# Optimization experiments

Hardware: AMD Instinct MI355X
Metric: run time of the kernel (lower is better)

## Reference

```python
import jax, jax.numpy as jnp
import numpy as np
import math

EPS = 1e-3  # numerical_stabilizer in relu_kernel_transformation


def setup_inputs() -> dict:
    key = jax.random.key(0)
    ks = jax.random.split(key, 6)
    B, L, DIM = 8, 4096, 768
    H, D, M = 12, 64, 256
    x = jax.random.normal(ks[0], (B, L, DIM), dtype=jnp.float32)
    qkv_w = jax.random.normal(ks[1], (3 * DIM, DIM), dtype=jnp.float32) * (DIM ** -0.5)
    qkv_b = jnp.zeros((3 * DIM,), dtype=jnp.float32)
    proj_w = jax.random.normal(ks[2], (DIM, DIM), dtype=jnp.float32) * (DIM ** -0.5)
    proj_b = jnp.zeros((DIM,), dtype=jnp.float32)
    # Gaussian orthogonal random matrix [M, D] (blocks of orthogonal rows, chi-scaled)
    blocks = []
    for i in range(M // D):
        g = jax.random.normal(ks[3 + 0] if False else jax.random.fold_in(ks[3], i), (D, D), dtype=jnp.float32)
        q, _ = jnp.linalg.qr(g)
        blocks.append(q.T)
    pm = jnp.concatenate(blocks, axis=0)  # [M, D]
    mult = jnp.linalg.norm(jax.random.normal(ks[4], (M, D), dtype=jnp.float32), axis=1)
    proj_mat = mult[:, None] * pm
    return {"x": x, "qkv_w": qkv_w, "qkv_b": qkv_b,
            "proj_w": proj_w, "proj_b": proj_b, "proj_mat": proj_mat}


def _relu_features(t, proj_mat):
    # t: [B, L, H, D], proj_mat: [M, D] -> [B, L, H, M]
    ratio = 1.0 / math.sqrt(float(proj_mat.shape[0]))
    z = ratio * jnp.einsum('blhd,md->blhm', t, proj_mat)
    return jax.nn.relu(z) + EPS


def reference(x, qkv_w, qkv_b, proj_w, proj_b, proj_mat):
    B, L, DIM = x.shape
    H = 12
    D = DIM // H
    qkv = x @ qkv_w.T + qkv_b                      # [B, L, 3*DIM]
    qkv = qkv.reshape(B, L, 3, H, D)
    q, k, v = qkv[:, :, 0], qkv[:, :, 1], qkv[:, :, 2]   # [B, L, H, D]
    q_p = _relu_features(q, proj_mat)              # [B, L, H, M]
    k_p = _relu_features(k, proj_mat)              # [B, L, H, M]
    # Non-causal FAVOR+ linear attention
    kv = jnp.einsum('blhm,blhd->bhmd', k_p, v)     # [B, H, M, D]
    k_sum = k_p.sum(axis=1)                        # [B, H, M]
    num = jnp.einsum('blhm,bhmd->blhd', q_p, kv)   # [B, L, H, D]
    den = jnp.einsum('blhm,bhm->blh', q_p, k_sum)  # [B, L, H]
    out = num / den[..., None]
    out = out.reshape(B, L, DIM)
    return out @ proj_w.T + proj_b
```

## Files before the change

kernel.cpp:

```cpp
#include <hip/hip_runtime.h>
#include <hip/hip_bf16.h>
#include <cstdint>

typedef __hip_bfloat16 bf16;
typedef short bf16x8 __attribute__((ext_vector_type(8)));
typedef float f32x4 __attribute__((ext_vector_type(4)));

#define RATIO 0.0625f
#define EPS_F 0.001f

__device__ __forceinline__ void unpack8(uint4 u, float* f) {
  f[0] = __uint_as_float(u.x << 16); f[1] = __uint_as_float(u.x & 0xffff0000u);
  f[2] = __uint_as_float(u.y << 16); f[3] = __uint_as_float(u.y & 0xffff0000u);
  f[4] = __uint_as_float(u.z << 16); f[5] = __uint_as_float(u.z & 0xffff0000u);
  f[6] = __uint_as_float(u.w << 16); f[7] = __uint_as_float(u.w & 0xffff0000u);
}

__device__ __forceinline__ unsigned short f2bf(float f) {
  unsigned int u = __float_as_uint(f);
  unsigned int r = (u + 0x7fffu + ((u >> 16) & 1u)) >> 16;
  return (unsigned short)r;
}

__device__ __forceinline__ void gload_lds16(const void* g, void* l) {
  __builtin_amdgcn_global_load_lds(
      (const __attribute__((address_space(1))) void*)(uintptr_t)g,
      (__attribute__((address_space(3))) void*)(uintptr_t)l, 16, 0, 0);
}

__global__ void conv_kernel(const float* __restrict__ src,
                            unsigned short* __restrict__ dst, long n) {
  long i = ((long)blockIdx.x * 256 + threadIdx.x) * 4;
  if (i < n) {
    float4 v = *(const float4*)(src + i);
    ushort4 o;
    o.x = f2bf(v.x); o.y = f2bf(v.y); o.z = f2bf(v.z); o.w = f2bf(v.w);
    *(ushort4*)(dst + i) = o;
  }
}

__device__ __forceinline__ void ds_read_B8(const short* Bb, int rB0, int l16,
                                           int quad, bf16x8 bfr[4][2]) {
  const int sw = l16 & 7;
#pragma unroll
  for (int ni = 0; ni < 4; ++ni)
#pragma unroll
    for (int ks = 0; ks < 2; ++ks)
      bfr[ni][ks] = *(const bf16x8*)
          &Bb[(rB0 + ni * 16 + l16) * 64 + (((ks * 4 + quad) ^ sw) * 8)];
}

template <int Q>
__device__ __forceinline__ void ds_read_A4(const short* Ab, int l16, int quad,
                                           bf16x8 af[2][2]) {
  const int sw = l16 & 7;
#pragma unroll
  for (int i = 0; i < 2; ++i)
#pragma unroll
    for (int ks = 0; ks < 2; ++ks)
      af[i][ks] = *(const bf16x8*)
          &Ab[((Q * 2 + i) * 16 + l16) * 64 + (((ks * 4 + quad) ^ sw) * 8)];
}

template <int Q>
__device__ __forceinline__ void mfma16(f32x4 acc[8][4], bf16x8 af[2][2],
                                       bf16x8 bfr[4][2]) {
#pragma unroll
  for (int i = 0; i < 2; ++i)
#pragma unroll
    for (int ni = 0; ni < 4; ++ni)
#pragma unroll
      for (int ks = 0; ks < 2; ++ks)
        acc[Q * 2 + i][ni] = __builtin_amdgcn_mfma_f32_16x16x32_bf16(
            af[i][ks], bfr[ni][ks], acc[Q * 2 + i][ni], 0, 0, 0);
}

template <bool OUT_F32>
__global__ __launch_bounds__(512, 2) void gemm_bt_kernel(
    const bf16* __restrict__ A, const bf16* __restrict__ Bt,
    const float* __restrict__ bias, void* __restrict__ Cout,
    int Ndim, int Kdim)
{
  __shared__ short lds[65536];
  const int tid = threadIdx.x;
  const int lane = tid & 63;
  const int w = tid >> 6;
  const int wr = w >> 2;
  const int wc = w & 3;
  const int quad = lane >> 4, l16 = lane & 15;

  int gx = gridDim.x;
  int nwg = gx * gridDim.y;
  int flat = blockIdx.y * gx + blockIdx.x;
  int qq = nwg >> 3, rr = nwg & 7;
  int xcd = flat & 7, sub = flat >> 3;
  int wg = (xcd < rr ? xcd * (qq + 1) : rr * (qq + 1) + (xcd - rr) * qq) + sub;
  long m0 = (long)(wg / gx) * 256;
  long n0 = (long)(wg % gx) * 256;

  const int r8 = lane >> 3;
  const int csw = ((lane & 7) ^ (r8 & 7)) * 8;
  const bf16* gAs = A + (m0 + (w >> 2) * 128 + (w & 3) * 8 + r8) * (long)Kdim + csw;
  const bf16* gBs = Bt + (n0 + w * 8 + r8) * (long)Kdim + csw;
  short* dA = &lds[(w >> 2) * 8192 + (w & 3) * 512];
  short* dB = &lds[32768 + w * 512];
  const long kb64 = 64L * Kdim;
  const long ka32 = 32L * Kdim;

  f32x4 acc[8][4];
#pragma unroll
  for (int i = 0; i < 8; i++)
#pragma unroll
    for (int j = 0; j < 4; j++)
      acc[i][j] = (f32x4){0.f, 0.f, 0.f, 0.f};

  const int NIT = Kdim >> 6;

#pragma unroll
  for (int j = 0; j < 4; ++j) gload_lds16(gBs + j * kb64, dB + j * 4096);
#pragma unroll
  for (int qa = 0; qa < 4; ++qa) gload_lds16(gAs + qa * ka32, dA + qa * 2048);
  asm volatile("s_waitcnt vmcnt(3)" ::: "memory");
  __builtin_amdgcn_s_barrier();

  bf16x8 bfr[4][2], af[2][2];

  for (int it = 0; it < NIT; ++it) {
    const int d = it & 1, nd = d ^ 1;
    const bool pf = (it < NIT - 1);
    const long kq1 = (long)(it + 1) * 64;
    const short* Ab = &lds[d * 16384 + wr * 8192];
    const short* Bb = &lds[32768 + d * 16384 + (wc >> 1) * 8192];
    const int rB0 = (wc & 1) * 64;
    short* dAn = dA + nd * 16384;
    short* dBn = dB + nd * 16384;

    ds_read_B8(Bb, rB0, l16, quad, bfr);
    ds_read_A4<0>(Ab, l16, quad, af);
    if (pf) {
      gload_lds16(gBs + kq1, dBn);
      gload_lds16(gBs + kb64 + kq1, dBn + 4096);
      asm volatile("s_waitcnt vmcnt(4)" ::: "memory");
    } else {
      asm volatile("s_waitcnt vmcnt(2)" ::: "memory");
    }
    asm volatile("s_waitcnt lgkmcnt(8)" ::: "memory");
    __builtin_amdgcn_s_barrier();
    asm volatile("s_waitcnt lgkmcnt(0)" ::: "memory");
    __builtin_amdgcn_sched_barrier(0);
    __builtin_amdgcn_s_setprio(1);
    mfma16<0>(acc, af, bfr);
    __builtin_amdgcn_s_setprio(0);
    __builtin_amdgcn_s_barrier();

    ds_read_A4<1>(Ab, l16, quad, af);
    if (pf) {
      gload_lds16(gBs + 2 * kb64 + kq1, dBn + 8192);
      gload_lds16(gBs + 3 * kb64 + kq1, dBn + 12288);
      asm volatile("s_waitcnt vmcnt(5)" ::: "memory");
    } else {
      asm volatile("s_waitcnt vmcnt(1)" ::: "memory");
    }
    __builtin_amdgcn_s_barrier();
    asm volatile("s_waitcnt lgkmcnt(0)" ::: "memory");
    __builtin_amdgcn_sched_barrier(0);
    __builtin_amdgcn_s_setprio(1);
    mfma16<1>(acc, af, bfr);
    __builtin_amdgcn_s_setprio(0);
    __builtin_amdgcn_s_barrier();

    ds_read_A4<2>(Ab, l16, quad, af);
    if (pf) {
      gload_lds16(gAs + kq1, dAn);
      gload_lds16(gAs + ka32 + kq1, dAn + 2048);
      asm volatile("s_waitcnt vmcnt(6)" ::: "memory");
    } else {
      asm volatile("s_waitcnt vmcnt(0)" ::: "memory");
    }
    __builtin_amdgcn_s_barrier();
    asm volatile("s_waitcnt lgkmcnt(0)" ::: "memory");
    __builtin_amdgcn_sched_barrier(0);
    __builtin_amdgcn_s_setprio(1);
    mfma16<2>(acc, af, bfr);
    __builtin_amdgcn_s_setprio(0);
    __builtin_amdgcn_s_barrier();

    ds_read_A4<3>(Ab, l16, quad, af);
    if (pf) {
      gload_lds16(gAs + 2 * ka32 + kq1, dAn + 4096);
      gload_lds16(gAs + 3 * ka32 + kq1, dAn + 6144);
      asm volatile("s_waitcnt vmcnt(3)" ::: "memory");
    }
    __builtin_amdgcn_s_barrier();
    asm volatile("s_waitcnt lgkmcnt(0)" ::: "memory");
    __builtin_amdgcn_sched_barrier(0);
    __builtin_amdgcn_s_setprio(1);
    mfma16<3>(acc, af, bfr);
    __builtin_amdgcn_s_setprio(0);
    __builtin_amdgcn_s_barrier();
  }

#pragma unroll
  for (int ni = 0; ni < 4; ++ni) {
    long col = n0 + wc * 64 + ni * 16 + l16;
    float bv = bias[col];
#pragma unroll
    for (int mi = 0; mi < 8; ++mi) {
      long row = m0 + wr * 128 + mi * 16 + quad * 4;
#pragma unroll
      for (int r = 0; r < 4; ++r) {
        float val = acc[mi][ni][r] + bv;
        if (OUT_F32)
          ((float*)Cout)[(row + r) * Ndim + col] = val;
        else
          ((bf16*)Cout)[(row + r) * Ndim + col] = __float2bfloat16(val);
      }
    }
  }
}

__global__ __launch_bounds__(256) void kv_mfma_kernel(
    const bf16* __restrict__ qkv, const bf16* __restrict__ pmb,
    float* __restrict__ kvbuf, float* __restrict__ ksumb)
{
  int bh = blockIdx.x;
  int b = bh / 12, h = bh % 12;
  int mb = blockIdx.y * 64;
  int tid = threadIdx.x, lane = tid & 63, w = tid >> 6;
  int quad = lane >> 4, l16 = lane & 15;

  __shared__ short k_lds[64 * 72];
  __shared__ short v_lds[64 * 72];
  __shared__ short kp3[64 * 72];
  __shared__ float red[4][64];

  bf16x8 bpm[4][2];
#pragma unroll
  for (int mt = 0; mt < 4; mt++)
#pragma unroll
    for (int ks = 0; ks < 2; ks++)
      bpm[mt][ks] = *(const bf16x8*)(pmb + (mb + mt * 16 + l16) * 64 + ks * 32 + quad * 8);

  f32x4 kvacc[4];
#pragma unroll
  for (int mt = 0; mt < 4; mt++) kvacc[mt] = (f32x4){0.f, 0.f, 0.f, 0.f};
  float ksum_r = 0.f;

  int srow = tid >> 2, sseg = (tid & 3) * 8;
  int swz = ((srow >> 3) & 3) << 4;
  int mm = tid & 63, lq = tid >> 6;

  for (int tile = 0; tile < 64; tile++) {
    long gr = ((long)(b * 4096 + tile * 64 + srow)) * 2304 + h * 64;
    uint4 kk0 = *(const uint4*)(qkv + gr + 768 + sseg);
    uint4 kk1 = *(const uint4*)(qkv + gr + 768 + sseg + 32);
    uint4 vv0 = *(const uint4*)(qkv + gr + 1536 + sseg);
    uint4 vv1 = *(const uint4*)(qkv + gr + 1536 + sseg + 32);
    __syncthreads();
    *(uint4*)&k_lds[srow * 72 + sseg] = kk0;
    *(uint4*)&k_lds[srow * 72 + sseg + 32] = kk1;
    *(uint4*)&v_lds[srow * 72 + (sseg ^ swz)] = vv0;
    *(uint4*)&v_lds[srow * 72 + ((sseg + 32) ^ swz)] = vv1;
    __syncthreads();

    {
      bf16x8 af[2];
#pragma unroll
      for (int ks = 0; ks < 2; ks++)
        af[ks] = *(const bf16x8*)&k_lds[(w * 16 + l16) * 72 + ks * 32 + quad * 8];
#pragma unroll
      for (int mt = 0; mt < 4; mt++) {
        f32x4 s = (f32x4){0.f, 0.f, 0.f, 0.f};
        s = __builtin_amdgcn_mfma_f32_16x16x32_bf16(af[0], bpm[mt][0], s, 0, 0, 0);
        s = __builtin_amdgcn_mfma_f32_16x16x32_bf16(af[1], bpm[mt][1], s, 0, 0, 0);
        ushort4 pk;
        pk.x = f2bf(fmaxf(s[0] * RATIO, 0.f) + EPS_F);
        pk.y = f2bf(fmaxf(s[1] * RATIO, 0.f) + EPS_F);
        pk.z = f2bf(fmaxf(s[2] * RATIO, 0.f) + EPS_F);
        pk.w = f2bf(fmaxf(s[3] * RATIO, 0.f) + EPS_F);
        *(ushort4*)&kp3[(mt * 16 + l16) * 72 + w * 16 + quad * 4] = pk;
      }
    }
    __syncthreads();

#pragma unroll
    for (int j = 0; j < 2; j++) {
      uint4 u = *(const uint4*)&kp3[mm * 72 + lq * 16 + j * 8];
      float f[8]; unpack8(u, f);
      ksum_r += ((f[0] + f[1]) + (f[2] + f[3])) + ((f[4] + f[5]) + (f[6] + f[7]));
    }

#pragma unroll
    for (int ls = 0; ls < 2; ls++) {
      bf16x8 a2[4];
#pragma unroll
      for (int mt = 0; mt < 4; mt++)
        a2[mt] = *(const bf16x8*)&kp3[(mt * 16 + l16) * 72 + ls * 32 + quad * 8];
      bf16x8 b2;
      int dcol = (w * 16 + l16) ^ (quad << 4);
#pragma unroll
      for (int jj = 0; jj < 8; jj++)
        b2[jj] = v_lds[(ls * 32 + quad * 8 + jj) * 72 + dcol];
#pragma unroll
      for (int mt = 0; mt < 4; mt++)
        kvacc[mt] = __builtin_amdgcn_mfma_f32_16x16x32_bf16(a2[mt], b2, kvacc[mt], 0, 0, 0);
    }
  }

#pragma unroll
  for (int mt = 0; mt < 4; mt++)
#pragma unroll
    for (int r = 0; r < 4; r++)
      kvbuf[(long)bh * 16384 + (w * 16 + l16) * 256 + mb + mt * 16 + quad * 4 + r] =
          kvacc[mt][r];

  red[lq][mm] = ksum_r;
  __syncthreads();
  if (tid < 64)
    ksumb[bh * 256 + mb + tid] =
        (red[0][tid] + red[1][tid]) + (red[2][tid] + red[3][tid]);
}

__global__ __launch_bounds__(256) void attn_mfma_kernel(
    const bf16* __restrict__ qkv, const bf16* __restrict__ pmb,
    const bf16* __restrict__ kvtb, const float* __restrict__ ksumb,
    bf16* __restrict__ attn)
{
  int bh = blockIdx.x;
  int b = bh / 12, h = bh % 12;
  int l0 = blockIdx.y * 64;
  int tid = threadIdx.x, lane = tid & 63, w = tid >> 6;
  int quad = lane >> 4, l16 = lane & 15;

  __shared__ short q_lds[64 * 72];
  __shared__ short qp2[64 * 264];
  __shared__ short kvt_lds[64 * 264];
  __shared__ float ksum_lds[256];
  __shared__ float den_part[4][64];

  {
    int srow = tid >> 2, sseg = (tid & 3) * 8;
    long gr = ((long)(b * 4096 + l0 + srow)) * 2304 + h * 64;
    *(uint4*)&q_lds[srow * 72 + sseg]      = *(const uint4*)(qkv + gr + sseg);
    *(uint4*)&q_lds[srow * 72 + sseg + 32] = *(const uint4*)(qkv + gr + sseg + 32);
  }
  {
    int row = tid >> 2, cb = (tid & 3) * 64;
    const bf16* src = kvtb + (long)bh * 16384 + row * 256 + cb;
    short* dst = &kvt_lds[row * 264 + cb];
#pragma unroll
    for (int j = 0; j < 8; j++)
      *(uint4*)(dst + j * 8) = *(const uint4*)(src + j * 8);
  }
  ksum_lds[tid] = ksumb[bh * 256 + tid];
  __syncthreads();

  {
    bf16x8 apm[4][2], bq[4][2];
#pragma unroll
    for (int mt = 0; mt < 4; mt++)
#pragma unroll
      for (int ks = 0; ks < 2; ks++)
        apm[mt][ks] = *(const bf16x8*)(pmb + (w * 64 + mt * 16 + l16) * 64 + ks * 32 + quad * 8);
#pragma unroll
    for (int lt = 0; lt < 4; lt++)
#pragma unroll
      for (int ks = 0; ks < 2; ks++)
        bq[lt][ks] = *(const bf16x8*)&q_lds[(lt * 16 + l16) * 72 + ks * 32 + quad * 8];

#pragma unroll
    for (int mt = 0; mt < 4; mt++)
#pragma unroll
      for (int lt = 0; lt < 4; lt++) {
        f32x4 s = (f32x4){0.f, 0.f, 0.f, 0.f};
        s = __builtin_amdgcn_mfma_f32_16x16x32_bf16(apm[mt][0], bq[lt][0], s, 0, 0, 0);
        s = __builtin_amdgcn_mfma_f32_16x16x32_bf16(apm[mt][1], bq[lt][1], s, 0, 0, 0);
        ushort4 pk;
        pk.x = f2bf(fmaxf(s[0] * RATIO, 0.f) + EPS_F);
        pk.y = f2bf(fmaxf(s[1] * RATIO, 0.f) + EPS_F);
        pk.z = f2bf(fmaxf(s[2] * RATIO, 0.f) + EPS_F);
        pk.w = f2bf(fmaxf(s[3] * RATIO, 0.f) + EPS_F);
        *(ushort4*)&qp2[(lt * 16 + l16) * 264 + w * 64 + mt * 16 + quad * 4] = pk;
      }
  }
  __syncthreads();

  {
    int l = tid & 63, Q = tid >> 6;
    float dp = 0.f;
#pragma unroll
    for (int j8 = 0; j8 < 8; j8++) {
      uint4 u = *(const uint4*)&qp2[l * 264 + Q * 64 + j8 * 8];
      float f[8]; unpack8(u, f);
#pragma unroll
      for (int i = 0; i < 8; i++) dp += f[i] * ksum_lds[Q * 64 + j8 * 8 + i];
    }
    den_part[Q][l] = dp;
  }

  f32x4 o[4];
#pragma unroll
  for (int dt = 0; dt < 4; dt++) o[dt] = (f32x4){0.f, 0.f, 0.f, 0.f};
#pragma unroll
  for (int ms = 0; ms < 8; ms++) {
    bf16x8 aq = *(const bf16x8*)&qp2[(w * 16 + l16) * 264 + ms * 32 + quad * 8];
#pragma unroll
    for (int dt = 0; dt < 4; dt++) {
      bf16x8 bk = *(const bf16x8*)&kvt_lds[(dt * 16 + l16) * 264 + ms * 32 + quad * 8];
      o[dt] = __builtin_amdgcn_mfma_f32_16x16x32_bf16(aq, bk, o[dt], 0, 0, 0);
    }
  }
  __syncthreads();

  float rden[4];
#pragma unroll
  for (int r = 0; r < 4; r++) {
    int l = w * 16 + quad * 4 + r;
    rden[r] = 1.f / (den_part[0][l] + den_part[1][l] + den_part[2][l] + den_part[3][l]);
  }
#pragma unroll
  for (int dt = 0; dt < 4; dt++)
#pragma unroll
    for (int r = 0; r < 4; r++) {
      int l = w * 16 + quad * 4 + r;
      attn[((long)(b * 4096 + l0 + l)) * 768 + h * 64 + dt * 16 + l16] =
          __float2bfloat16(o[dt][r] * rden[r]);
    }
}

extern "C" void kernel_launch(void* const* d_in, const int* in_sizes, int n_in,
                              void* d_out, int out_size, void* d_ws, size_t ws_size,
                              hipStream_t stream)
{
  const float* x      = (const float*)d_in[0];
  const float* qkv_w  = (const float*)d_in[1];
  const float* qkv_b  = (const float*)d_in[2];
  const float* proj_w = (const float*)d_in[3];
  const float* proj_b = (const float*)d_in[4];
  const float* pmat   = (const float*)d_in[5];
  float* out = (float*)d_out;

  char* ws = (char*)d_ws;
  bf16*  qkv   = (bf16*)ws;
  bf16*  xbuf  = (bf16*)(ws + 150994944);
  bf16*  attn  = xbuf;
  float* kvbuf = (float*)(ws + 201326592);
  float* ksumb = (float*)(ws + 207618048);
  bf16*  wqkv  = (bf16*)(ws + 207716352);
  bf16*  kvtb  = (bf16*)(ws + 207716352);
  bf16*  pmb   = (bf16*)(ws + 210862080);
  bf16*  wproj = (bf16*)(ws + 211255296);

  conv_kernel<<<dim3(25165824 / 1024), 256, 0, stream>>>(x, (unsigned short*)xbuf, 25165824L);
  conv_kernel<<<dim3(1769472 / 1024), 256, 0, stream>>>(qkv_w, (unsigned short*)wqkv, 1769472L);
  conv_kernel<<<dim3(589824 / 1024), 256, 0, stream>>>(proj_w, (unsigned short*)wproj, 589824L);

  gemm_bt_kernel<false><<<dim3(2304 / 256, 32768 / 256), 512, 0, stream>>>(
      xbuf, wqkv, qkv_b, qkv, 2304, 768);

  conv_kernel<<<dim3(16384 / 1024), 256, 0, stream>>>(pmat, (unsigned short*)pmb, 16384L);

  kv_mfma_kernel<<<dim3(96, 4), 256, 0, stream>>>(qkv, pmb, kvbuf, ksumb);

  conv_kernel<<<dim3(1572864 / 1024), 256, 0, stream>>>(kvbuf, (unsigned short*)kvtb, 1572864L);

  attn_mfma_kernel<<<dim3(96, 64), 256, 0, stream>>>(qkv, pmb, kvtb, ksumb, attn);

  gemm_bt_kernel<true><<<dim3(768 / 256, 32768 / 256), 512, 0, stream>>>(
      attn, wproj, proj_b, out, 768, 768);
}
```

Measured before the change: 561.0 us.

## Split KV reduction over sequence halves and prefetch next K/V tile

The kv_mfma kernel now runs over two halves of the sequence via a z grid dimension, doubling the block count from 384 to 768, and writes two partial KV and k_sum buffers. A new kv_add kernel sums the partials and converts KV to bf16, replacing the plain conversion pass. The K/V global loads for the next tile are also issued early, during the current tile's compute, so their latency overlaps with MFMA work. The cost is an extra partial buffer round-trip through memory, with the second partial stored in the reused xbuf region.

```diff
diff --git a/kernel.cpp b/kernel.cpp
--- a/kernel.cpp
+++ b/kernel.cpp
@@ -36,6 +36,28 @@
     ushort4 o;
     o.x = f2bf(v.x); o.y = f2bf(v.y); o.z = f2bf(v.z); o.w = f2bf(v.w);
     *(ushort4*)(dst + i) = o;
+  }
+}
+
+__global__ void kv_add_kernel(const float* __restrict__ a,
+                              const float* __restrict__ b,
+                              unsigned short* __restrict__ kvtb,
+                              float* __restrict__ ks_a,
+                              const float* __restrict__ ks_b) {
+  long i4 = ((long)blockIdx.x * 256 + threadIdx.x) * 4;
+  if (i4 < 1572864) {
+    float4 x = *(const float4*)(a + i4);
+    float4 y = *(const float4*)(b + i4);
+    ushort4 o;
+    o.x = f2bf(x.x + y.x); o.y = f2bf(x.y + y.y);
+    o.z = f2bf(x.z + y.z); o.w = f2bf(x.w + y.w);
+    *(ushort4*)(kvtb + i4) = o;
+  }
+  if (i4 < 24576) {
+    float4 p = *(const float4*)(ks_a + i4);
+    float4 q = *(const float4*)(ks_b + i4);
+    p.x += q.x; p.y += q.y; p.z += q.z; p.w += q.w;
+    *(float4*)(ks_a + i4) = p;
   }
 }
 
@@ -221,11 +243,16 @@
 
 __global__ __launch_bounds__(256) void kv_mfma_kernel(
     const bf16* __restrict__ qkv, const bf16* __restrict__ pmb,
-    float* __restrict__ kvbuf, float* __restrict__ ksumb)
+    float* __restrict__ kvp0, float* __restrict__ kvp1,
+    float* __restrict__ ksp0, float* __restrict__ ksp1)
 {
   int bh = blockIdx.x;
   int b = bh / 12, h = bh % 12;
   int mb = blockIdx.y * 64;
+  int zh = blockIdx.z;
+  float* kvout = zh ? kvp1 : kvp0;
+  float* ksout = zh ? ksp1 : ksp0;
+  int l0 = zh * 2048;
   int tid = threadIdx.x, lane = tid & 63, w = tid >> 6;
   int quad = lane >> 4, l16 = lane & 15;
 
@@ -250,12 +277,13 @@
   int swz = ((srow >> 3) & 3) << 4;
   int mm = tid & 63, lq = tid >> 6;
 
-  for (int tile = 0; tile < 64; tile++) {
-    long gr = ((long)(b * 4096 + tile * 64 + srow)) * 2304 + h * 64;
-    uint4 kk0 = *(const uint4*)(qkv + gr + 768 + sseg);
-    uint4 kk1 = *(const uint4*)(qkv + gr + 768 + sseg + 32);
-    uint4 vv0 = *(const uint4*)(qkv + gr + 1536 + sseg);
-    uint4 vv1 = *(const uint4*)(qkv + gr + 1536 + sseg + 32);
+  long gr = ((long)(b * 4096 + l0 + srow)) * 2304 + h * 64;
+  uint4 kk0 = *(const uint4*)(qkv + gr + 768 + sseg);
+  uint4 kk1 = *(const uint4*)(qkv + gr + 768 + sseg + 32);
+  uint4 vv0 = *(const uint4*)(qkv + gr + 1536 + sseg);
+  uint4 vv1 = *(const uint4*)(qkv + gr + 1536 + sseg + 32);
+
+  for (int tile = 0; tile < 32; tile++) {
     __syncthreads();
     *(uint4*)&k_lds[srow * 72 + sseg] = kk0;
     *(uint4*)&k_lds[srow * 72 + sseg + 32] = kk1;
@@ -281,6 +309,14 @@
         *(ushort4*)&kp3[(mt * 16 + l16) * 72 + w * 16 + quad * 4] = pk;
       }
     }
+
+    if (tile < 31) {
+      long g2 = ((long)(b * 4096 + l0 + (tile + 1) * 64 + srow)) * 2304 + h * 64;
+      kk0 = *(const uint4*)(qkv + g2 + 768 + sseg);
+      kk1 = *(const uint4*)(qkv + g2 + 768 + sseg + 32);
+      vv0 = *(const uint4*)(qkv + g2 + 1536 + sseg);
+      vv1 = *(const uint4*)(qkv + g2 + 1536 + sseg + 32);
+    }
     __syncthreads();
 
 #pragma unroll
@@ -311,13 +347,13 @@
   for (int mt = 0; mt < 4; mt++)
 #pragma unroll
     for (int r = 0; r < 4; r++)
-      kvbuf[(long)bh * 16384 + (w * 16 + l16) * 256 + mb + mt * 16 + quad * 4 + r] =
+      kvout[(long)bh * 16384 + (w * 16 + l16) * 256 + mb + mt * 16 + quad * 4 + r] =
           kvacc[mt][r];
 
   red[lq][mm] = ksum_r;
   __syncthreads();
   if (tid < 64)
-    ksumb[bh * 256 + mb + tid] =
+    ksout[bh * 256 + mb + tid] =
         (red[0][tid] + red[1][tid]) + (red[2][tid] + red[3][tid]);
 }
 
@@ -444,8 +480,11 @@
   bf16*  qkv   = (bf16*)ws;
   bf16*  xbuf  = (bf16*)(ws + 150994944);
   bf16*  attn  = xbuf;
-  float* kvbuf = (float*)(ws + 201326592);
-  float* ksumb = (float*)(ws + 207618048);
+  float* kvp1  = (float*)(ws + 150994944);
+  float* ksp1  = (float*)(ws + 157286400);
+  float* kvp0  = (float*)(ws + 201326592);
+  float* ksp0  = (float*)(ws + 207618048);
+  float* ksumb = ksp0;
   bf16*  wqkv  = (bf16*)(ws + 207716352);
   bf16*  kvtb  = (bf16*)(ws + 207716352);
   bf16*  pmb   = (bf16*)(ws + 210862080);
@@ -460,9 +499,9 @@
 
   conv_kernel<<<dim3(16384 / 1024), 256, 0, stream>>>(pmat, (unsigned short*)pmb, 16384L);
 
-  kv_mfma_kernel<<<dim3(96, 4), 256, 0, stream>>>(qkv, pmb, kvbuf, ksumb);
-
-  conv_kernel<<<dim3(1572864 / 1024), 256, 0, stream>>>(kvbuf, (unsigned short*)kvtb, 1572864L);
+  kv_mfma_kernel<<<dim3(96, 4, 2), 256, 0, stream>>>(qkv, pmb, kvp0, kvp1, ksp0, ksp1);
+
+  kv_add_kernel<<<dim3(1536), 256, 0, stream>>>(kvp0, kvp1, (unsigned short*)kvtb, ksp0, ksp1);
 
   attn_mfma_kernel<<<dim3(96, 64), 256, 0, stream>>>(qkv, pmb, kvtb, ksumb, attn);
 
```

After: 541.6 us. 3.5% less time.
